# Kernel optimization log

Hardware: AMD Instinct MI355X
Metric: run time of the kernel (lower is better)

Reference implementation:

```python
import jax, jax.numpy as jnp
import numpy as np

NUM_TOKENS = 8192
CODEBOOK_DIM = 64
BETA = 0.25
DECAY = 0.99
EPS = 1e-05
B, C, H, W = 32, 64, 32, 32


def setup_inputs() -> dict:
    key = jax.random.key(0)
    k1, k2, k3, k4 = jax.random.split(key, 4)
    z = jax.random.normal(k1, (B, C, H, W), dtype=jnp.float32)
    emb = jax.random.normal(k2, (NUM_TOKENS, CODEBOOK_DIM), dtype=jnp.float32)
    ema_w = jax.random.normal(k3, (NUM_TOKENS, CODEBOOK_DIM), dtype=jnp.float32)
    cluster_size = jax.random.uniform(k4, (NUM_TOKENS,), dtype=jnp.float32)
    return {"z": z, "emb": emb, "ema_w": ema_w, "cluster_size": cluster_size}


def reference(z, emb, ema_w, cluster_size):
    # NCHW -> NHWC, flatten to [N, D]
    z_nhwc = jnp.transpose(z, (0, 2, 3, 1))
    z_flat = z_nhwc.reshape(-1, CODEBOOK_DIM)  # [N, D]

    # squared distances: ||z||^2 + ||e||^2 - 2 z e^T  -> [N, K]
    d = (jnp.sum(z_flat * z_flat, axis=1, keepdims=True)
         + jnp.sum(emb * emb, axis=1)
         - 2.0 * jnp.einsum('nd,kd->nk', z_flat, emb))
    idx = jnp.argmin(d, axis=1)  # [N] int

    z_q = emb[idx].reshape(z_nhwc.shape)  # gather + reshape

    # EMA updates (training-mode buffer math); one-hot matmuls expressed as segment sums
    new_cluster = jax.ops.segment_sum(jnp.ones_like(idx, dtype=z.dtype), idx, num_segments=NUM_TOKENS)
    cs = DECAY * cluster_size + (1.0 - DECAY) * new_cluster
    new_ema_w = jax.ops.segment_sum(z_flat, idx, num_segments=NUM_TOKENS)
    ema_w_out = DECAY * ema_w + (1.0 - DECAY) * new_ema_w
    cs_sum = jnp.sum(cs)
    cs_norm = (cs + EPS) / (cs_sum + NUM_TOKENS * EPS)
    emb_out = ema_w_out / cs_norm[:, None]

    # commitment loss uses z_q from the OLD codebook (as in torch code)
    loss = BETA * jnp.mean((jax.lax.stop_gradient(z_q) - z_nhwc) ** 2)

    # straight-through estimator, back to NCHW
    z_q_st = z_nhwc + jax.lax.stop_gradient(z_q - z_nhwc)
    z_q_st = jnp.transpose(z_q_st, (0, 3, 1, 2))
    return z_q_st, loss, idx, cs_norm, ema_w_out, emb_out
```

## Files before the change

### kernel.cpp

```cpp
#include <hip/hip_runtime.h>
#include <float.h>

#define N_TOK   32768
#define DIM     64
#define K_CODES 8192
#define HWSZ    1024
#define CHW     65536
#define NELEM   2097152

typedef short  bf16x8 __attribute__((ext_vector_type(8)));
typedef float  f32x16 __attribute__((ext_vector_type(16)));

static __device__ __forceinline__ unsigned short f2bf(float x) {
    unsigned u = __float_as_uint(x);
    unsigned r = u + 0x7FFFu + ((u >> 16) & 1u);
    return (unsigned short)(r >> 16);
}
static __device__ __forceinline__ float bf2f(unsigned short h) {
    return __uint_as_float(((unsigned)h) << 16);
}

__global__ __launch_bounds__(256) void prep_e(const float* __restrict__ emb,
                                              unsigned short* __restrict__ blob,
                                              float* __restrict__ eng,
                                              unsigned long long* __restrict__ packed,
                                              int* __restrict__ cnt_i,
                                              float* __restrict__ sums) {
    __shared__ float part[512];
    const int gid = blockIdx.x * 256 + threadIdx.x;
    packed[gid] = ~0ull;
    if (gid < K_CODES) cnt_i[gid] = 0;
    if (gid < 2) sums[gid] = 0.f;

    int tile = blockIdx.x;
    #pragma unroll
    for (int u0 = 0; u0 < 2; ++u0) {
        int u = threadIdx.x + u0 * 256;
        int s = u >> 7, h = (u >> 6) & 1, n = u & 63;
        const float* src = emb + (tile * 64 + n) * 64 + s * 16 + h * 8;
        float4 v0 = *(const float4*)src;
        float4 v1 = *(const float4*)(src + 4);
        float x[8] = {v0.x, v0.y, v0.z, v0.w, v1.x, v1.y, v1.z, v1.w};
        unsigned short hi[8], lo[8];
        float ss = 0.f;
        #pragma unroll
        for (int j = 0; j < 8; ++j) {
            hi[j] = f2bf(x[j]);
            lo[j] = f2bf(x[j] - bf2f(hi[j]));
            ss += x[j] * x[j];
        }
        part[u] = ss;
        unsigned short* dhi = blob + (size_t)tile * 8192 + ((s * 2 + 0) * 2 + h) * 512 + n * 8;
        unsigned short* dlo = blob + (size_t)tile * 8192 + ((s * 2 + 1) * 2 + h) * 512 + n * 8;
        uint4 ph, pl;
        ph.x = (unsigned)hi[0] | ((unsigned)hi[1] << 16);
        ph.y = (unsigned)hi[2] | ((unsigned)hi[3] << 16);
        ph.z = (unsigned)hi[4] | ((unsigned)hi[5] << 16);
        ph.w = (unsigned)hi[6] | ((unsigned)hi[7] << 16);
        pl.x = (unsigned)lo[0] | ((unsigned)lo[1] << 16);
        pl.y = (unsigned)lo[2] | ((unsigned)lo[3] << 16);
        pl.z = (unsigned)lo[4] | ((unsigned)lo[5] << 16);
        pl.w = (unsigned)lo[6] | ((unsigned)lo[7] << 16);
        *(uint4*)dhi = ph;
        *(uint4*)dlo = pl;
    }
    __syncthreads();
    if (threadIdx.x < 64) {
        float s = 0.f;
        #pragma unroll
        for (int j = 0; j < 8; ++j) s += part[threadIdx.x + j * 64];
        eng[tile * 64 + threadIdx.x] = s;
    }
}

__global__ __launch_bounds__(256, 3) void vq_argmin(const float* __restrict__ z,
                                                    const unsigned short* __restrict__ blob,
                                                    const float* __restrict__ eng,
                                                    unsigned long long* __restrict__ packed) {
    __shared__ __align__(16) unsigned short zh[64 * 72];
    __shared__ __align__(16) unsigned short zl[64 * 72];
    __shared__ unsigned long long red[64 * 4];

    const int tid  = threadIdx.x;
    const int lane = tid & 63;
    const int wid  = tid >> 6;
    const int l31  = lane & 31, h = lane >> 5;

    const int tb = blockIdx.x & 511;
    const int ks = blockIdx.x >> 9;
    const int n0 = tb * 64;
    const int zbase = (n0 >> 10) * CHW + (n0 & 1023);

    {
        int f4 = tid & 15;
        int c0 = tid >> 4;
        #pragma unroll
        for (int r = 0; r < 4; ++r) {
            int c = c0 * 4 + r;
            float4 v = *(const float4*)(z + zbase + c * HWSZ + f4 * 4);
            float x[4] = {v.x, v.y, v.z, v.w};
            #pragma unroll
            for (int e = 0; e < 4; ++e) {
                int t = f4 * 4 + e;
                float xs = -2.0f * x[e];
                unsigned short hi = f2bf(xs);
                zh[t * 72 + c] = hi;
                zl[t * 72 + c] = f2bf(xs - bf2f(hi));
            }
        }
    }
    __syncthreads();

    bf16x8 T0h[4], T0l[4], T1h[4], T1l[4];
    {
        int r0 = l31;
        int r1 = 32 + l31;
        #pragma unroll
        for (int s = 0; s < 4; ++s) {
            T0h[s] = *(const bf16x8*)(&zh[r0 * 72 + s * 16 + h * 8]);
            T0l[s] = *(const bf16x8*)(&zl[r0 * 72 + s * 16 + h * 8]);
            T1h[s] = *(const bf16x8*)(&zh[r1 * 72 + s * 16 + h * 8]);
            T1l[s] = *(const bf16x8*)(&zl[r1 * 72 + s * 16 + h * 8]);
        }
    }

    const int hk0 = ks * 128 + wid;
    const unsigned short* bp = blob + (size_t)(hk0 >> 1) * 8192 + ((hk0 & 1) * 32 + l31) * 8;
    const float* ep = eng + (hk0 >> 1) * 64 + (hk0 & 1) * 32 + 4 * h;
    int scode = __builtin_amdgcn_readfirstlane((hk0 >> 1) * 64 + (hk0 & 1) * 32);

    bf16x8 Eh[4], El[4];
    #pragma unroll
    for (int s = 0; s < 4; ++s) {
        Eh[s] = *(const bf16x8*)(bp + (4 * s + h) * 512);
        El[s] = *(const bf16x8*)(bp + (4 * s + 2 + h) * 512);
    }
    float4 g0 = *(const float4*)(ep);
    float4 g1 = *(const float4*)(ep + 8);
    float4 g2 = *(const float4*)(ep + 16);
    float4 g3 = *(const float4*)(ep + 24);

    float minv0 = FLT_MAX, minv1 = FLT_MAX;
    int   mini0 = 0,       mini1 = 0;

    for (int i = 0; i < 32; ++i) {
        f32x16 ac0, ac1;
        ac0[0]  = g0.x; ac0[1]  = g0.y; ac0[2]  = g0.z; ac0[3]  = g0.w;
        ac0[4]  = g1.x; ac0[5]  = g1.y; ac0[6]  = g1.z; ac0[7]  = g1.w;
        ac0[8]  = g2.x; ac0[9]  = g2.y; ac0[10] = g2.z; ac0[11] = g2.w;
        ac0[12] = g3.x; ac0[13] = g3.y; ac0[14] = g3.z; ac0[15] = g3.w;
        ac1 = ac0;

        ep += 128;
        g0 = *(const float4*)(ep);
        g1 = *(const float4*)(ep + 8);
        g2 = *(const float4*)(ep + 16);
        g3 = *(const float4*)(ep + 24);

        __builtin_amdgcn_s_setprio(1);
        #pragma unroll
        for (int s = 0; s < 4; ++s) {
            ac0 = __builtin_amdgcn_mfma_f32_32x32x16_bf16(El[s], T0h[s], ac0, 0, 0, 0);
            ac1 = __builtin_amdgcn_mfma_f32_32x32x16_bf16(El[s], T1h[s], ac1, 0, 0, 0);
            ac0 = __builtin_amdgcn_mfma_f32_32x32x16_bf16(Eh[s], T0l[s], ac0, 0, 0, 0);
            ac1 = __builtin_amdgcn_mfma_f32_32x32x16_bf16(Eh[s], T1l[s], ac1, 0, 0, 0);
            ac0 = __builtin_amdgcn_mfma_f32_32x32x16_bf16(Eh[s], T0h[s], ac0, 0, 0, 0);
            ac1 = __builtin_amdgcn_mfma_f32_32x32x16_bf16(Eh[s], T1h[s], ac1, 0, 0, 0);
        }
        __builtin_amdgcn_s_setprio(0);

        bp += 2 * 8192;
        #pragma unroll
        for (int s = 0; s < 4; ++s) {
            Eh[s] = *(const bf16x8*)(bp + (4 * s + h) * 512);
            El[s] = *(const bf16x8*)(bp + (4 * s + 2 + h) * 512);
        }

        #pragma unroll
        for (int r = 0; r < 16; ++r) {
            int code = scode + ((r & 3) + 8 * (r >> 2));
            if (ac0[r] < minv0) { minv0 = ac0[r]; mini0 = code; }
            if (ac1[r] < minv1) { minv1 = ac1[r]; mini1 = code; }
        }
        scode += 128;
    }
    mini0 += 4 * h;
    mini1 += 4 * h;

    unsigned u0 = __float_as_uint(minv0);
    u0 = (u0 & 0x80000000u) ? ~u0 : (u0 | 0x80000000u);
    unsigned long long k0 = ((unsigned long long)u0 << 32) | (unsigned)mini0;
    unsigned u1 = __float_as_uint(minv1);
    u1 = (u1 & 0x80000000u) ? ~u1 : (u1 | 0x80000000u);
    unsigned long long k1 = ((unsigned long long)u1 << 32) | (unsigned)mini1;
    unsigned long long o0 = __shfl_xor(k0, 32, 64);
    if (o0 < k0) k0 = o0;
    unsigned long long o1 = __shfl_xor(k1, 32, 64);
    if (o1 < k1) k1 = o1;
    if (h == 0) {
        red[l31 * 4 + wid]        = k0;
        red[(32 + l31) * 4 + wid] = k1;
    }
    __syncthreads();
    if (tid < 64) {
        unsigned long long a = red[tid * 4], b = red[tid * 4 + 1];
        unsigned long long c = red[tid * 4 + 2], d = red[tid * 4 + 3];
        unsigned long long m = (b < a) ? b : a;
        if (c < m) m = c;
        if (d < m) m = d;
        atomicMin(&packed[n0 + tid], m);
    }
}

__global__ __launch_bounds__(256) void zq_loss(const float* __restrict__ z,
                                               const float* __restrict__ emb,
                                               const float* __restrict__ ema_w,
                                               const unsigned long long* __restrict__ packed,
                                               float* __restrict__ zq_out,
                                               float* __restrict__ idx_out,
                                               int* __restrict__ idx_i32,
                                               int* __restrict__ cnt_i,
                                               float* __restrict__ loss_sum,
                                               float* __restrict__ z_t,
                                               float* __restrict__ emao_out) {
    __shared__ float e_lds[64][68];
    __shared__ float z_lds[64][68];

    const int tid = threadIdx.x;
    const int n0  = blockIdx.x * 64;
    const int t   = tid >> 2, q = tid & 3;
    const int n   = n0 + t;
    const int b   = n0 >> 10;
    const int hw0 = n0 & 1023;
    const int zb  = b * CHW + hw0;

    const int idx = (int)(packed[n] & 0xFFFFFFFFull);
    if (q == 0) {
        idx_out[n] = (float)idx;
        idx_i32[n] = idx;
        atomicAdd(&cnt_i[idx], 1);
    }
    {
        int g = blockIdx.x * 256 + tid;
        #pragma unroll
        for (int j = 0; j < 4; ++j) {
            int i = g + j * 131072;
            emao_out[i] = 0.99f * ema_w[i];
        }
    }
    {
        const float* er = emb + idx * 64 + q * 16;
        float4 e0 = *(const float4*)er,       e1 = *(const float4*)(er + 4);
        float4 e2 = *(const float4*)(er + 8), e3 = *(const float4*)(er + 12);
        *(float4*)&e_lds[t][q * 16]      = e0;
        *(float4*)&e_lds[t][q * 16 + 4]  = e1;
        *(float4*)&e_lds[t][q * 16 + 8]  = e2;
        *(float4*)&e_lds[t][q * 16 + 12] = e3;
    }
    {
        const int f4 = tid & 15, c0 = tid >> 4;
        #pragma unroll
        for (int r = 0; r < 4; ++r) {
            int c = c0 * 4 + r;
            float4 v = *(const float4*)(z + zb + c * HWSZ + f4 * 4);
            z_lds[f4 * 4 + 0][c] = v.x;
            z_lds[f4 * 4 + 1][c] = v.y;
            z_lds[f4 * 4 + 2][c] = v.z;
            z_lds[f4 * 4 + 3][c] = v.w;
        }
    }
    __syncthreads();

    if (z_t) {
        #pragma unroll
        for (int u = 0; u < 4; ++u)
            *(float4*)&z_t[n * 64 + q * 16 + u * 4] = *(float4*)&z_lds[t][q * 16 + u * 4];
    }
    {
        const int f4 = tid & 15, c0 = tid >> 4;
        #pragma unroll
        for (int r = 0; r < 4; ++r) {
            int c = c0 * 4 + r;
            float4 o;
            { float zv = z_lds[f4*4+0][c]; o.x = zv + (e_lds[f4*4+0][c] - zv); }
            { float zv = z_lds[f4*4+1][c]; o.y = zv + (e_lds[f4*4+1][c] - zv); }
            { float zv = z_lds[f4*4+2][c]; o.z = zv + (e_lds[f4*4+2][c] - zv); }
            { float zv = z_lds[f4*4+3][c]; o.w = zv + (e_lds[f4*4+3][c] - zv); }
            *(float4*)(zq_out + zb + c * HWSZ + f4 * 4) = o;
        }
    }
    float lsum = 0.f;
    #pragma unroll
    for (int j = 0; j < 16; ++j) {
        int c = q * 16 + j;
        float dd = e_lds[t][c] - z_lds[t][c];
        lsum += dd * dd;
    }
    #pragma unroll
    for (int m = 32; m >= 1; m >>= 1) lsum += __shfl_xor(lsum, m, 64);
    if ((tid & 63) == 0) atomicAdd(loss_sum, lsum);
}

__global__ __launch_bounds__(1024) void scan_cs(const int* __restrict__ cnt_i,
                                                const float* __restrict__ csize,
                                                const float* __restrict__ loss_sum,
                                                int* __restrict__ cursor,
                                                float* __restrict__ csn_out,
                                                float* __restrict__ loss_out) {
    __shared__ int   sc[1024];
    __shared__ float sf[1024];
    const int tid = threadIdx.x;
    int v[8], part = 0;
    float cv[8], fpart = 0.f;
    #pragma unroll
    for (int j = 0; j < 8; ++j) { v[j] = cnt_i[tid * 8 + j]; part += v[j]; }
    #pragma unroll
    for (int j = 0; j < 8; ++j) {
        cv[j] = 0.99f * csize[tid * 8 + j] + 0.01f * (float)v[j];
        fpart += cv[j];
    }
    sc[tid] = part;
    sf[tid] = fpart;
    __syncthreads();
    for (int off = 1; off < 1024; off <<= 1) {
        int add = (tid >= off) ? sc[tid - off] : 0;
        __syncthreads();
        sc[tid] += add;
        __syncthreads();
    }
    int run = sc[tid] - part;
    #pragma unroll
    for (int j = 0; j < 8; ++j) {
        cursor[tid * 8 + j] = run;
        run += v[j];
    }
    for (int off = 512; off >= 1; off >>= 1) {
        if (tid < off) sf[tid] += sf[tid + off];
        __syncthreads();
    }
    float denom = sf[0] + (float)(K_CODES * 1e-5);
    #pragma unroll
    for (int j = 0; j < 8; ++j) csn_out[tid * 8 + j] = (cv[j] + 1e-5f) / denom;
    if (tid == 0) *loss_out = 0.25f * (*loss_sum) * (1.0f / (float)NELEM);
}

__global__ __launch_bounds__(256) void scatter_kernel(const int* __restrict__ idx_i32,
                                                      int* __restrict__ cursor,
                                                      int* __restrict__ tok_of,
                                                      int* __restrict__ code_of) {
    int t = blockIdx.x * 256 + threadIdx.x;
    int k = idx_i32[t];
    int pos = atomicAdd(&cursor[k], 1);
    tok_of[pos] = t;
    code_of[pos] = k;
}

__global__ __launch_bounds__(256) void ema_acc(const float* __restrict__ z,
                                               const float* __restrict__ z_t,
                                               const int* __restrict__ tok_of,
                                               const int* __restrict__ code_of,
                                               float* __restrict__ emao_out) {
    const int wv   = (blockIdx.x * 256 + threadIdx.x) >> 6;
    const int lane = threadIdx.x & 63;
    const int pos0 = wv * 64;
    const int tok  = tok_of[pos0 + lane];
    const int cod  = code_of[pos0 + lane];
    float acc = 0.f;
    #pragma unroll
    for (int g = 0; g < 8; ++g) {
        int tk[8], kk[8];
        #pragma unroll
        for (int j = 0; j < 8; ++j) {
            tk[j] = __shfl(tok, g * 8 + j, 64);
            kk[j] = __shfl(cod, g * 8 + j, 64);
        }
        float v[8];
        if (z_t) {
            #pragma unroll
            for (int j = 0; j < 8; ++j) v[j] = z_t[tk[j] * 64 + lane];
        } else {
            #pragma unroll
            for (int j = 0; j < 8; ++j)
                v[j] = z[(tk[j] >> 10) * CHW + lane * HWSZ + (tk[j] & 1023)];
        }
        int knext = (g < 7) ? __shfl(cod, g * 8 + 8, 64) : -1;
        #pragma unroll
        for (int j = 0; j < 8; ++j) {
            acc += v[j];
            int kn = (j < 7) ? kk[j + 1] : knext;
            if (kn != kk[j]) {
                atomicAdd(&emao_out[kk[j] * 64 + lane], 0.01f * acc);
                acc = 0.f;
            }
        }
    }
}

__global__ __launch_bounds__(256) void final_div(const float* __restrict__ emao_out,
                                                 const float* __restrict__ csn_out,
                                                 float* __restrict__ embo_out) {
    int g = blockIdx.x * 256 + threadIdx.x;
    embo_out[g] = emao_out[g] / csn_out[g >> 6];
}

extern "C" void kernel_launch(void* const* d_in, const int* in_sizes, int n_in,
                              void* d_out, int out_size, void* d_ws, size_t ws_size,
                              hipStream_t stream) {
    (void)in_sizes; (void)n_in; (void)out_size;
    const float* z     = (const float*)d_in[0];
    const float* emb   = (const float*)d_in[1];
    const float* ema_w = (const float*)d_in[2];
    const float* csize = (const float*)d_in[3];

    float* out      = (float*)d_out;
    float* zq_out   = out;
    float* loss_out = out + 2097152;
    float* idx_out  = out + 2097153;
    float* csn_out  = out + 2129921;
    float* emao_out = out + 2138113;
    float* embo_out = out + 2662401;

    char* wsb = (char*)d_ws;
    unsigned short*     blob    = (unsigned short*)(wsb);
    float*              eng     = (float*)(wsb + 2097152);
    unsigned long long* packed  = (unsigned long long*)(wsb + 2129920);
    int*                code_of = (int*)(wsb + 2129920);
    int*                idx_i32 = (int*)(wsb + 2392064);
    int*                cnt_i   = (int*)(wsb + 2523136);
    float*              sums    = (float*)(wsb + 2555904);
    int*                cursor  = (int*)(wsb + 2555920);
    int*                tok_of  = (int*)(wsb + 2588688);
    const size_t zt_off = 2719760;
    float* z_t = (ws_size >= zt_off + (size_t)NELEM * 4) ? (float*)(wsb + zt_off) : nullptr;

    prep_e<<<128, 256, 0, stream>>>(emb, blob, eng, packed, cnt_i, sums);
    vq_argmin<<<1024, 256, 0, stream>>>(z, blob, eng, packed);
    zq_loss<<<N_TOK / 64, 256, 0, stream>>>(z, emb, ema_w, packed, zq_out, idx_out,
                                            idx_i32, cnt_i, sums + 1, z_t, emao_out);
    scan_cs<<<1, 1024, 0, stream>>>(cnt_i, csize, sums + 1, cursor, csn_out, loss_out);
    scatter_kernel<<<N_TOK / 256, 256, 0, stream>>>(idx_i32, cursor, tok_of, code_of);
    ema_acc<<<128, 256, 0, stream>>>(z, z_t, tok_of, code_of, emao_out);
    final_div<<<K_CODES * DIM / 256, 256, 0, stream>>>(emao_out, csn_out, embo_out);
}
```

Measured before the change: 216.5 us.

## Fuse EMA segment-sum into zq_loss via direct atomics, drop sort-based accumulation

The counting-sort pipeline is removed: the cursor prefix scan in scan_cs, scatter_kernel, ema_acc and the z_t transpose buffer. In its place each zq_loss block issues per-token atomicAdds of 0.01*z into emao_out, taking z from the LDS tile it already holds. The 0.99*ema_w initialisation moves into prep_e so it finishes before the atomics begin. This saves two launches and a full write and read of the z transpose, at the cost of about 2M uncoalesced float atomics, which may contend on codes that many tokens pick.

```diff
diff --git a/kernel.cpp b/kernel.cpp
--- a/kernel.cpp
+++ b/kernel.cpp
@@ -21,16 +21,24 @@
 }
 
 __global__ __launch_bounds__(256) void prep_e(const float* __restrict__ emb,
+                                              const float* __restrict__ ema_w,
                                               unsigned short* __restrict__ blob,
                                               float* __restrict__ eng,
                                               unsigned long long* __restrict__ packed,
                                               int* __restrict__ cnt_i,
-                                              float* __restrict__ sums) {
+                                              float* __restrict__ sums,
+                                              float* __restrict__ emao_out) {
     __shared__ float part[512];
     const int gid = blockIdx.x * 256 + threadIdx.x;
     packed[gid] = ~0ull;
     if (gid < K_CODES) cnt_i[gid] = 0;
     if (gid < 2) sums[gid] = 0.f;
+
+    #pragma unroll
+    for (int j = 0; j < 16; ++j) {
+        int i = gid + j * 32768;
+        emao_out[i] = 0.99f * ema_w[i];
+    }
 
     int tile = blockIdx.x;
     #pragma unroll
@@ -214,14 +222,12 @@
 
 __global__ __launch_bounds__(256) void zq_loss(const float* __restrict__ z,
                                                const float* __restrict__ emb,
-                                               const float* __restrict__ ema_w,
                                                const unsigned long long* __restrict__ packed,
                                                float* __restrict__ zq_out,
                                                float* __restrict__ idx_out,
                                                int* __restrict__ idx_i32,
                                                int* __restrict__ cnt_i,
                                                float* __restrict__ loss_sum,
-                                               float* __restrict__ z_t,
                                                float* __restrict__ emao_out) {
     __shared__ float e_lds[64][68];
     __shared__ float z_lds[64][68];
@@ -230,6 +236,7 @@
     const int n0  = blockIdx.x * 64;
     const int t   = tid >> 2, q = tid & 3;
     const int n   = n0 + t;
+    const int w   = tid >> 6, lane = tid & 63;
     const int b   = n0 >> 10;
     const int hw0 = n0 & 1023;
     const int zb  = b * CHW + hw0;
@@ -239,14 +246,6 @@
         idx_out[n] = (float)idx;
         idx_i32[n] = idx;
         atomicAdd(&cnt_i[idx], 1);
-    }
-    {
-        int g = blockIdx.x * 256 + tid;
-        #pragma unroll
-        for (int j = 0; j < 4; ++j) {
-            int i = g + j * 131072;
-            emao_out[i] = 0.99f * ema_w[i];
-        }
     }
     {
         const float* er = emb + idx * 64 + q * 16;
@@ -271,11 +270,13 @@
     }
     __syncthreads();
 
-    if (z_t) {
-        #pragma unroll
-        for (int u = 0; u < 4; ++u)
-            *(float4*)&z_t[n * 64 + q * 16 + u * 4] = *(float4*)&z_lds[t][q * 16 + u * 4];
-    }
+    #pragma unroll
+    for (int u = 0; u < 16; ++u) {
+        int tt = w * 16 + u;
+        int ix = __shfl(idx, u * 4, 64);
+        atomicAdd(&emao_out[ix * 64 + lane], 0.01f * z_lds[tt][lane]);
+    }
+
     {
         const int f4 = tid & 15, c0 = tid >> 4;
         #pragma unroll
@@ -304,36 +305,21 @@
 __global__ __launch_bounds__(1024) void scan_cs(const int* __restrict__ cnt_i,
                                                 const float* __restrict__ csize,
                                                 const float* __restrict__ loss_sum,
-                                                int* __restrict__ cursor,
                                                 float* __restrict__ csn_out,
                                                 float* __restrict__ loss_out) {
-    __shared__ int   sc[1024];
     __shared__ float sf[1024];
     const int tid = threadIdx.x;
-    int v[8], part = 0;
+    int v[8];
     float cv[8], fpart = 0.f;
     #pragma unroll
-    for (int j = 0; j < 8; ++j) { v[j] = cnt_i[tid * 8 + j]; part += v[j]; }
+    for (int j = 0; j < 8; ++j) v[j] = cnt_i[tid * 8 + j];
     #pragma unroll
     for (int j = 0; j < 8; ++j) {
         cv[j] = 0.99f * csize[tid * 8 + j] + 0.01f * (float)v[j];
         fpart += cv[j];
     }
-    sc[tid] = part;
     sf[tid] = fpart;
     __syncthreads();
-    for (int off = 1; off < 1024; off <<= 1) {
-        int add = (tid >= off) ? sc[tid - off] : 0;
-        __syncthreads();
-        sc[tid] += add;
-        __syncthreads();
-    }
-    int run = sc[tid] - part;
-    #pragma unroll
-    for (int j = 0; j < 8; ++j) {
-        cursor[tid * 8 + j] = run;
-        run += v[j];
-    }
     for (int off = 512; off >= 1; off >>= 1) {
         if (tid < off) sf[tid] += sf[tid + off];
         __syncthreads();
@@ -342,58 +328,6 @@
     #pragma unroll
     for (int j = 0; j < 8; ++j) csn_out[tid * 8 + j] = (cv[j] + 1e-5f) / denom;
     if (tid == 0) *loss_out = 0.25f * (*loss_sum) * (1.0f / (float)NELEM);
-}
-
-__global__ __launch_bounds__(256) void scatter_kernel(const int* __restrict__ idx_i32,
-                                                      int* __restrict__ cursor,
-                                                      int* __restrict__ tok_of,
-                                                      int* __restrict__ code_of) {
-    int t = blockIdx.x * 256 + threadIdx.x;
-    int k = idx_i32[t];
-    int pos = atomicAdd(&cursor[k], 1);
-    tok_of[pos] = t;
-    code_of[pos] = k;
-}
-
-__global__ __launch_bounds__(256) void ema_acc(const float* __restrict__ z,
-                                               const float* __restrict__ z_t,
-                                               const int* __restrict__ tok_of,
-                                               const int* __restrict__ code_of,
-                                               float* __restrict__ emao_out) {
-    const int wv   = (blockIdx.x * 256 + threadIdx.x) >> 6;
-    const int lane = threadIdx.x & 63;
-    const int pos0 = wv * 64;
-    const int tok  = tok_of[pos0 + lane];
-    const int cod  = code_of[pos0 + lane];
-    float acc = 0.f;
-    #pragma unroll
-    for (int g = 0; g < 8; ++g) {
-        int tk[8], kk[8];
-        #pragma unroll
-        for (int j = 0; j < 8; ++j) {
-            tk[j] = __shfl(tok, g * 8 + j, 64);
-            kk[j] = __shfl(cod, g * 8 + j, 64);
-        }
-        float v[8];
-        if (z_t) {
-            #pragma unroll
-            for (int j = 0; j < 8; ++j) v[j] = z_t[tk[j] * 64 + lane];
-        } else {
-            #pragma unroll
-            for (int j = 0; j < 8; ++j)
-                v[j] = z[(tk[j] >> 10) * CHW + lane * HWSZ + (tk[j] & 1023)];
-        }
-        int knext = (g < 7) ? __shfl(cod, g * 8 + 8, 64) : -1;
-        #pragma unroll
-        for (int j = 0; j < 8; ++j) {
-            acc += v[j];
-            int kn = (j < 7) ? kk[j + 1] : knext;
-            if (kn != kk[j]) {
-                atomicAdd(&emao_out[kk[j] * 64 + lane], 0.01f * acc);
-                acc = 0.f;
-            }
-        }
-    }
 }
 
 __global__ __launch_bounds__(256) void final_div(const float* __restrict__ emao_out,
@@ -406,7 +340,7 @@
 extern "C" void kernel_launch(void* const* d_in, const int* in_sizes, int n_in,
                               void* d_out, int out_size, void* d_ws, size_t ws_size,
                               hipStream_t stream) {
-    (void)in_sizes; (void)n_in; (void)out_size;
+    (void)in_sizes; (void)n_in; (void)out_size; (void)ws_size;
     const float* z     = (const float*)d_in[0];
     const float* emb   = (const float*)d_in[1];
     const float* ema_w = (const float*)d_in[2];
@@ -424,21 +358,14 @@
     unsigned short*     blob    = (unsigned short*)(wsb);
     float*              eng     = (float*)(wsb + 2097152);
     unsigned long long* packed  = (unsigned long long*)(wsb + 2129920);
-    int*                code_of = (int*)(wsb + 2129920);
     int*                idx_i32 = (int*)(wsb + 2392064);
     int*                cnt_i   = (int*)(wsb + 2523136);
     float*              sums    = (float*)(wsb + 2555904);
-    int*                cursor  = (int*)(wsb + 2555920);
-    int*                tok_of  = (int*)(wsb + 2588688);
-    const size_t zt_off = 2719760;
-    float* z_t = (ws_size >= zt_off + (size_t)NELEM * 4) ? (float*)(wsb + zt_off) : nullptr;
-
-    prep_e<<<128, 256, 0, stream>>>(emb, blob, eng, packed, cnt_i, sums);
+
+    prep_e<<<128, 256, 0, stream>>>(emb, ema_w, blob, eng, packed, cnt_i, sums, emao_out);
     vq_argmin<<<1024, 256, 0, stream>>>(z, blob, eng, packed);
-    zq_loss<<<N_TOK / 64, 256, 0, stream>>>(z, emb, ema_w, packed, zq_out, idx_out,
-                                            idx_i32, cnt_i, sums + 1, z_t, emao_out);
-    scan_cs<<<1, 1024, 0, stream>>>(cnt_i, csize, sums + 1, cursor, csn_out, loss_out);
-    scatter_kernel<<<N_TOK / 256, 256, 0, stream>>>(idx_i32, cursor, tok_of, code_of);
-    ema_acc<<<128, 256, 0, stream>>>(z, z_t, tok_of, code_of, emao_out);
+    zq_loss<<<N_TOK / 64, 256, 0, stream>>>(z, emb, packed, zq_out, idx_out,
+                                            idx_i32, cnt_i, sums + 1, emao_out);
+    scan_cs<<<1, 1024, 0, stream>>>(cnt_i, csize, sums + 1, csn_out, loss_out);
     final_div<<<K_CODES * DIM / 256, 256, 0, stream>>>(emao_out, csn_out, embo_out);
 }
```

Result: faster. 201.2 us (-7.0%).
